# Kernel tuning notes

Hardware: AMD Instinct MI355X
Metric: run time of the kernel (lower is better)

## Reference

```python
import jax, jax.numpy as jnp
import numpy as np

B, S, IN_F, OUT_F, RANK = 4, 4096, 4096, 4096, 64

def soft_threshold24(w):
    # 2:4 soft-threshold pruning: groups of 4 along last dim; keep top-2 |w|,
    # soft-threshold by t = 3rd-largest |w| in each group: sign(w)*relu(|w|-t).
    g = w.reshape(w.shape[0], -1, 4)
    a = jnp.abs(g)
    t = jnp.sort(a, axis=-1)[..., 1:2]  # 3rd largest = 2nd smallest of 4
    s = jnp.sign(g) * jnp.maximum(a - t, 0.0)
    return s.reshape(w.shape)

def fake_fp8_mm(a, b):
    # simulated fp8 GEMM per fake_fp8_mm: fp16 operands, fp32 accumulate/output
    return jnp.matmul(a.astype(jnp.float16), b.astype(jnp.float16),
                      preferred_element_type=jnp.float32)

def setup_inputs():
    key = jax.random.key(0)
    k1, k2, k3 = jax.random.split(key, 3)
    x = jax.random.normal(k1, (B, S, IN_F), jnp.float32)
    std_a = float(np.sqrt(2.0 / (IN_F + RANK)))   # xavier_normal_
    std_b = float(np.sqrt(2.0 / (OUT_F + RANK)))
    weight_A = jax.random.normal(k2, (IN_F, RANK), jnp.float32) * std_a
    weight_B = jax.random.normal(k3, (OUT_F, RANK), jnp.float32) * std_b
    bias = jnp.zeros((OUT_F,), jnp.float32)
    scale_A = jnp.float32(1.0)
    scale_B = jnp.float32(1.0)
    return {"x": x, "weight_A": weight_A, "weight_B": weight_B,
            "bias": bias, "scale_A": scale_A, "scale_B": scale_B}

def reference(x, weight_A, weight_B, bias, scale_A, scale_B):
    wA = soft_threshold24(weight_A) * scale_A      # [IN, R], 2:4 sparse along R
    wB = soft_threshold24(weight_B) * scale_B      # [OUT, R], 2:4 sparse along R
    xf = x.reshape(-1, x.shape[-1])                # [N, IN]
    x_proj = fake_fp8_mm(xf, wA)                   # [N, R]   == FP8SparseOp(x, wA.T, None)
    out = fake_fp8_mm(x_proj, wB.T) + bias         # [N, OUT] == FP8SparseOp(x_proj, wB, bias)
    return out.reshape(*x.shape[:-1], OUT_F)
```

## Files before the change

### kernel.cpp

```cpp
#include <hip/hip_runtime.h>
#include <hip/hip_cooperative_groups.h>

namespace cg = cooperative_groups;

#define IN_FEAT 4096
#define OUT_FEAT 4096
#define RANK 64
#define NROWS 16384
#define TM 32
#define BT 512
#define KC 256
#define WA_STRIDE 264
#define XP_STRIDE 72
#define PART_STRIDE 68

typedef _Float16 half_t;
typedef _Float16 f16x4 __attribute__((ext_vector_type(4)));
typedef _Float16 f16x8 __attribute__((ext_vector_type(8)));
typedef float f32x4 __attribute__((ext_vector_type(4)));

__device__ __forceinline__ f16x4 thr4(float4 v, float s) {
    float a0 = fabsf(v.x), a1 = fabsf(v.y), a2 = fabsf(v.z), a3 = fabsf(v.w);
    float lo1 = fminf(a0, a1), hi1 = fmaxf(a0, a1);
    float lo2 = fminf(a2, a3), hi2 = fmaxf(a2, a3);
    float t = fminf(fmaxf(lo1, lo2), fminf(hi1, hi2));
    f16x4 r;
    r[0] = (half_t)(copysignf(fmaxf(a0 - t, 0.0f), v.x) * s);
    r[1] = (half_t)(copysignf(fmaxf(a1 - t, 0.0f), v.y) * s);
    r[2] = (half_t)(copysignf(fmaxf(a2 - t, 0.0f), v.z) * s);
    r[3] = (half_t)(copysignf(fmaxf(a3 - t, 0.0f), v.w) * s);
    return r;
}

__global__ __launch_bounds__(512) void coop_kernel(
    const float* __restrict__ x, const float* __restrict__ wA,
    const float* __restrict__ wB, const float* __restrict__ bias,
    const float* __restrict__ scaleA, const float* __restrict__ scaleB,
    float* __restrict__ out, half_t* __restrict__ wAT, half_t* __restrict__ wBh)
{
    __shared__ float xp_part[4][TM][PART_STRIDE];
    __shared__ __align__(16) half_t xp[TM][XP_STRIDE];

    int tid = threadIdx.x;
    int bid = blockIdx.x;

    {
        int id = bid * BT + tid;
        if (id < 131072) {
            bool isB = id >= 65536;
            int gid = id & 65535;
            int row = gid >> 4;
            int gq  = gid & 15;
            const float* src = (isB ? wB : wA) + (size_t)row * RANK + gq * 4;
            float s = isB ? scaleB[0] : scaleA[0];
            f16x4 h = thr4(*(const float4*)src, s);
            if (!isB) {
                int c = gq * 4;
                wAT[(size_t)(c + 0) * IN_FEAT + row] = h[0];
                wAT[(size_t)(c + 1) * IN_FEAT + row] = h[1];
                wAT[(size_t)(c + 2) * IN_FEAT + row] = h[2];
                wAT[(size_t)(c + 3) * IN_FEAT + row] = h[3];
            } else {
                *(f16x4*)(wBh + (size_t)row * RANK + gq * 4) = h;
            }
        }
    }
    cg::this_grid().sync();

    int wave = tid >> 6;
    int lane = tid & 63;
    int l16  = lane & 15;
    int g    = lane >> 4;
    int rowbase = bid * TM;
    int stripe  = wave & 1;
    int ks      = wave >> 1;

    {
        const float* xrow = x + (size_t)(rowbase + stripe * 16 + l16) * IN_FEAT;
        int kbeg = ks * (IN_FEAT / 4);
        f32x4 acc[4] = {f32x4{0,0,0,0}, f32x4{0,0,0,0}, f32x4{0,0,0,0}, f32x4{0,0,0,0}};

#pragma unroll 2
        for (int k0 = kbeg; k0 < kbeg + IN_FEAT / 4; k0 += 32) {
            float4 xa = *(const float4*)(xrow + k0 + 8 * g);
            float4 xb = *(const float4*)(xrow + k0 + 8 * g + 4);
            f16x8 a;
            a[0] = (half_t)xa.x; a[1] = (half_t)xa.y; a[2] = (half_t)xa.z; a[3] = (half_t)xa.w;
            a[4] = (half_t)xb.x; a[5] = (half_t)xb.y; a[6] = (half_t)xb.z; a[7] = (half_t)xb.w;
#pragma unroll
            for (int f = 0; f < 4; ++f) {
                f16x8 b = *(const f16x8*)(wAT + (size_t)(16 * f + l16) * IN_FEAT + k0 + 8 * g);
                acc[f] = __builtin_amdgcn_mfma_f32_16x16x32_f16(a, b, acc[f], 0, 0, 0);
            }
        }
#pragma unroll
        for (int f = 0; f < 4; ++f)
#pragma unroll
            for (int r = 0; r < 4; ++r)
                xp_part[ks][stripe * 16 + 4 * g + r][16 * f + l16] = acc[f][r];
    }
    __syncthreads();

#pragma unroll
    for (int i = 0; i < (TM * RANK) / BT; ++i) {
        int e = i * BT + tid;
        int r = e >> 6, c = e & 63;
        xp[r][c] = (half_t)((xp_part[0][r][c] + xp_part[1][r][c]) +
                            (xp_part[2][r][c] + xp_part[3][r][c]));
    }
    __syncthreads();

    {
        const half_t* xprow = &xp[stripe * 16 + l16][0];
        f16x8 a0 = *(const f16x8*)(xprow + 8 * g);
        f16x8 a1 = *(const f16x8*)(xprow + 32 + 8 * g);

        int cb0 = ks * (OUT_FEAT / 4);
        for (int cb = cb0; cb < cb0 + OUT_FEAT / 4; cb += 64) {
#pragma unroll
            for (int f = 0; f < 4; ++f) {
                int col = cb + 16 * f + l16;
                const half_t* wp = wBh + (size_t)col * RANK;
                f16x8 b0 = *(const f16x8*)(wp + 8 * g);
                f16x8 b1 = *(const f16x8*)(wp + 32 + 8 * g);
                f32x4 acc2 = {0, 0, 0, 0};
                acc2 = __builtin_amdgcn_mfma_f32_16x16x32_f16(a0, b0, acc2, 0, 0, 0);
                acc2 = __builtin_amdgcn_mfma_f32_16x16x32_f16(a1, b1, acc2, 0, 0, 0);
                float bv = bias[col];
#pragma unroll
                for (int r = 0; r < 4; ++r)
                    __builtin_nontemporal_store(acc2[r] + bv,
                        &out[(size_t)(rowbase + stripe * 16 + 4 * g + r) * OUT_FEAT + col]);
            }
        }
    }
}

__global__ __launch_bounds__(256) void fused_kernel(
    const float* __restrict__ x, const float* __restrict__ wA,
    const float* __restrict__ wB, const float* __restrict__ bias,
    const float* __restrict__ scaleA, const float* __restrict__ scaleB,
    float* __restrict__ out)
{
    __shared__ __align__(16) half_t wAsT[RANK][WA_STRIDE];
    __shared__ float xp_part[2][TM][XP_STRIDE];
    __shared__ __align__(16) half_t xp[TM][XP_STRIDE];

    int tid  = threadIdx.x;
    int wave = tid >> 6;
    int lane = tid & 63;
    int l16  = lane & 15;
    int g    = lane >> 4;
    int rowbase = blockIdx.x * TM;
    int stripe  = wave & 1;
    int ks      = wave >> 1;

    float sA = scaleA[0];
    float sB = scaleB[0];

    const float* xrow = x + (size_t)(rowbase + stripe * 16 + l16) * IN_FEAT;
    f32x4 acc[4] = {f32x4{0,0,0,0}, f32x4{0,0,0,0}, f32x4{0,0,0,0}, f32x4{0,0,0,0}};

    for (int chunk = 0; chunk < IN_FEAT / KC; ++chunk) {
        int k0 = chunk * KC;
#pragma unroll
        for (int pp = 0; pp < 2; ++pp) {
            int p = tid + pp * 256;
            int q = p & 15;
            int r = p >> 4;
            f16x8 vc0, vc1, vc2, vc3;
#pragma unroll
            for (int i = 0; i < 8; ++i) {
                float4 v = *(const float4*)(wA + (size_t)(k0 + 8 * r + i) * RANK + 4 * q);
                f16x4 h = thr4(v, sA);
                vc0[i] = h[0]; vc1[i] = h[1]; vc2[i] = h[2]; vc3[i] = h[3];
            }
            *(f16x8*)&wAsT[4 * q + 0][8 * r] = vc0;
            *(f16x8*)&wAsT[4 * q + 1][8 * r] = vc1;
            *(f16x8*)&wAsT[4 * q + 2][8 * r] = vc2;
            *(f16x8*)&wAsT[4 * q + 3][8 * r] = vc3;
        }
        __syncthreads();

#pragma unroll
        for (int it = 0; it < 4; ++it) {
            int kloc = ks * 128 + it * 32;
            float4 xa = *(const float4*)(xrow + k0 + kloc + 8 * g);
            float4 xb = *(const float4*)(xrow + k0 + kloc + 8 * g + 4);
            f16x8 a;
            a[0] = (half_t)xa.x; a[1] = (half_t)xa.y; a[2] = (half_t)xa.z; a[3] = (half_t)xa.w;
            a[4] = (half_t)xb.x; a[5] = (half_t)xb.y; a[6] = (half_t)xb.z; a[7] = (half_t)xb.w;
#pragma unroll
            for (int f = 0; f < 4; ++f) {
                f16x8 b = *(const f16x8*)&wAsT[16 * f + l16][kloc + 8 * g];
                acc[f] = __builtin_amdgcn_mfma_f32_16x16x32_f16(a, b, acc[f], 0, 0, 0);
            }
        }
        __syncthreads();
    }

#pragma unroll
    for (int f = 0; f < 4; ++f)
#pragma unroll
        for (int r = 0; r < 4; ++r)
            xp_part[ks][stripe * 16 + 4 * g + r][16 * f + l16] = acc[f][r];
    __syncthreads();

#pragma unroll
    for (int i = 0; i < (TM * RANK) / 256; ++i) {
        int e = i * 256 + tid;
        int r = e >> 6, c = e & 63;
        xp[r][c] = (half_t)(xp_part[0][r][c] + xp_part[1][r][c]);
    }
    __syncthreads();

    {
        const half_t* xprow = &xp[stripe * 16 + l16][0];
        f16x8 a0 = *(const f16x8*)(xprow + 8 * g);
        f16x8 a1 = *(const f16x8*)(xprow + 32 + 8 * g);

        int cb0 = ks * (OUT_FEAT / 2);
        for (int cb = cb0; cb < cb0 + OUT_FEAT / 2; cb += 16) {
            int col = cb + l16;
            const float* wp = wB + (size_t)col * RANK;
            float4 w00 = *(const float4*)(wp + 8 * g);
            float4 w01 = *(const float4*)(wp + 8 * g + 4);
            float4 w10 = *(const float4*)(wp + 32 + 8 * g);
            float4 w11 = *(const float4*)(wp + 32 + 8 * g + 4);
            f16x4 b00 = thr4(w00, sB), b01 = thr4(w01, sB);
            f16x4 b10 = thr4(w10, sB), b11 = thr4(w11, sB);
            f16x8 b0, b1;
            b0[0]=b00[0]; b0[1]=b00[1]; b0[2]=b00[2]; b0[3]=b00[3];
            b0[4]=b01[0]; b0[5]=b01[1]; b0[6]=b01[2]; b0[7]=b01[3];
            b1[0]=b10[0]; b1[1]=b10[1]; b1[2]=b10[2]; b1[3]=b10[3];
            b1[4]=b11[0]; b1[5]=b11[1]; b1[6]=b11[2]; b1[7]=b11[3];

            f32x4 acc2 = {0, 0, 0, 0};
            acc2 = __builtin_amdgcn_mfma_f32_16x16x32_f16(a0, b0, acc2, 0, 0, 0);
            acc2 = __builtin_amdgcn_mfma_f32_16x16x32_f16(a1, b1, acc2, 0, 0, 0);
            float bv = bias[col];
#pragma unroll
            for (int r = 0; r < 4; ++r)
                out[(size_t)(rowbase + stripe * 16 + 4 * g + r) * OUT_FEAT + col] = acc2[r] + bv;
        }
    }
}

extern "C" void kernel_launch(void* const* d_in, const int* in_sizes, int n_in,
                              void* d_out, int out_size, void* d_ws, size_t ws_size,
                              hipStream_t stream) {
    const float* x      = (const float*)d_in[0];
    const float* wA     = (const float*)d_in[1];
    const float* wB     = (const float*)d_in[2];
    const float* bias   = (const float*)d_in[3];
    const float* scaleA = (const float*)d_in[4];
    const float* scaleB = (const float*)d_in[5];
    float* out = (float*)d_out;

    const size_t WS_NEED = (size_t)RANK * IN_FEAT * 2
                         + (size_t)OUT_FEAT * RANK * 2;

    if (ws_size >= WS_NEED && d_ws != nullptr) {
        half_t* wAT = (half_t*)d_ws;
        half_t* wBh = wAT + (size_t)RANK * IN_FEAT;
        void* args[] = {(void*)&x, (void*)&wA, (void*)&wB, (void*)&bias,
                        (void*)&scaleA, (void*)&scaleB, (void*)&out,
                        (void*)&wAT, (void*)&wBh};
        hipLaunchCooperativeKernel((void*)coop_kernel, dim3(NROWS / TM), dim3(BT),
                                   args, 0, stream);
    } else {
        fused_kernel<<<NROWS / TM, 256, 0, stream>>>(x, wA, wB, bias, scaleA, scaleB, out);
    }
}
```

Before: 239.5 us.

## Stage x through double-buffered LDS and split first GEMM by output columns

The first GEMM now loads each x row tile cooperatively into a double-buffered fp16 LDS buffer with register prefetch. Each wave computes one 16-column slice of the rank over the full K range, where before four K-split partials were reduced through LDS. This removes the redundant per-wave global x loads and the fp32 partial reduction. The cost is a block barrier per 256-wide K chunk. The change also swaps nontemporal output stores for plain stores, unrolls the second GEMM loop, and falls back to the non-cooperative kernel if the cooperative launch fails.

```diff
diff --git a/kernel.cpp b/kernel.cpp
--- a/kernel.cpp
+++ b/kernel.cpp
@@ -9,10 +9,11 @@
 #define NROWS 16384
 #define TM 32
 #define BT 512
+#define KC2 256
+#define SXS 264
+#define XP_STRIDE 72
 #define KC 256
 #define WA_STRIDE 264
-#define XP_STRIDE 72
-#define PART_STRIDE 68
 
 typedef _Float16 half_t;
 typedef _Float16 f16x4 __attribute__((ext_vector_type(4)));
@@ -32,13 +33,20 @@
     return r;
 }
 
-__global__ __launch_bounds__(512) void coop_kernel(
+__device__ __forceinline__ f16x4 cvt4(f32x4 v) {
+    f16x4 h;
+    h[0] = (half_t)v[0]; h[1] = (half_t)v[1];
+    h[2] = (half_t)v[2]; h[3] = (half_t)v[3];
+    return h;
+}
+
+__global__ __launch_bounds__(BT) void coop_kernel(
     const float* __restrict__ x, const float* __restrict__ wA,
     const float* __restrict__ wB, const float* __restrict__ bias,
     const float* __restrict__ scaleA, const float* __restrict__ scaleB,
     float* __restrict__ out, half_t* __restrict__ wAT, half_t* __restrict__ wBh)
 {
-    __shared__ float xp_part[4][TM][PART_STRIDE];
+    __shared__ __align__(16) half_t xs[2][TM][SXS];
     __shared__ __align__(16) half_t xp[TM][XP_STRIDE];
 
     int tid = threadIdx.x;
@@ -73,40 +81,57 @@
     int g    = lane >> 4;
     int rowbase = bid * TM;
     int stripe  = wave & 1;
-    int ks      = wave >> 1;
+    int quad    = wave >> 1;
+
+    int srow = tid >> 4;
+    int sseg = tid & 15;
+    const float* srcrow = x + (size_t)(rowbase + srow) * IN_FEAT + sseg * 4;
+
+    f32x4 ld0, ld1, ld2, ld3;
 
     {
-        const float* xrow = x + (size_t)(rowbase + stripe * 16 + l16) * IN_FEAT;
-        int kbeg = ks * (IN_FEAT / 4);
-        f32x4 acc[4] = {f32x4{0,0,0,0}, f32x4{0,0,0,0}, f32x4{0,0,0,0}, f32x4{0,0,0,0}};
-
-#pragma unroll 2
-        for (int k0 = kbeg; k0 < kbeg + IN_FEAT / 4; k0 += 32) {
-            float4 xa = *(const float4*)(xrow + k0 + 8 * g);
-            float4 xb = *(const float4*)(xrow + k0 + 8 * g + 4);
-            f16x8 a;
-            a[0] = (half_t)xa.x; a[1] = (half_t)xa.y; a[2] = (half_t)xa.z; a[3] = (half_t)xa.w;
-            a[4] = (half_t)xb.x; a[5] = (half_t)xb.y; a[6] = (half_t)xb.z; a[7] = (half_t)xb.w;
-#pragma unroll
-            for (int f = 0; f < 4; ++f) {
-                f16x8 b = *(const f16x8*)(wAT + (size_t)(16 * f + l16) * IN_FEAT + k0 + 8 * g);
-                acc[f] = __builtin_amdgcn_mfma_f32_16x16x32_f16(a, b, acc[f], 0, 0, 0);
-            }
-        }
-#pragma unroll
-        for (int f = 0; f < 4; ++f)
-#pragma unroll
-            for (int r = 0; r < 4; ++r)
-                xp_part[ks][stripe * 16 + 4 * g + r][16 * f + l16] = acc[f][r];
-    }
-    __syncthreads();
-
-#pragma unroll
-    for (int i = 0; i < (TM * RANK) / BT; ++i) {
-        int e = i * BT + tid;
-        int r = e >> 6, c = e & 63;
-        xp[r][c] = (half_t)((xp_part[0][r][c] + xp_part[1][r][c]) +
-                            (xp_part[2][r][c] + xp_part[3][r][c]));
+        {
+            const f32x4* p = (const f32x4*)(srcrow);
+            ld0 = p[0]; ld1 = p[16]; ld2 = p[32]; ld3 = p[48];
+            half_t* dst = &xs[0][srow][sseg * 4];
+            *(f16x4*)(dst +   0) = cvt4(ld0);
+            *(f16x4*)(dst +  64) = cvt4(ld1);
+            *(f16x4*)(dst + 128) = cvt4(ld2);
+            *(f16x4*)(dst + 192) = cvt4(ld3);
+        }
+        __syncthreads();
+
+        f32x4 acc = {0, 0, 0, 0};
+        const half_t* wcol = wAT + (size_t)(quad * 16 + l16) * IN_FEAT;
+        const half_t* arow = &xs[0][stripe * 16 + l16][0];
+        const int xsstep = TM * SXS;
+
+        for (int c = 0; c < IN_FEAT / KC2; ++c) {
+            if (c + 1 < IN_FEAT / KC2) {
+                const f32x4* p = (const f32x4*)(srcrow + (c + 1) * KC2);
+                ld0 = p[0]; ld1 = p[16]; ld2 = p[32]; ld3 = p[48];
+            }
+            int kb = c * KC2;
+            const half_t* ar = arow + (c & 1) * xsstep;
+#pragma unroll
+            for (int k8 = 0; k8 < KC2 / 32; ++k8) {
+                f16x8 a = *(const f16x8*)(ar + k8 * 32 + 8 * g);
+                f16x8 b = *(const f16x8*)(wcol + kb + k8 * 32 + 8 * g);
+                acc = __builtin_amdgcn_mfma_f32_16x16x32_f16(a, b, acc, 0, 0, 0);
+            }
+            if (c + 1 < IN_FEAT / KC2) {
+                half_t* dst = &xs[(c + 1) & 1][srow][sseg * 4];
+                *(f16x4*)(dst +   0) = cvt4(ld0);
+                *(f16x4*)(dst +  64) = cvt4(ld1);
+                *(f16x4*)(dst + 128) = cvt4(ld2);
+                *(f16x4*)(dst + 192) = cvt4(ld3);
+            }
+            __syncthreads();
+        }
+
+#pragma unroll
+        for (int r = 0; r < 4; ++r)
+            xp[stripe * 16 + 4 * g + r][quad * 16 + l16] = (half_t)acc[r];
     }
     __syncthreads();
 
@@ -115,7 +140,8 @@
         f16x8 a0 = *(const f16x8*)(xprow + 8 * g);
         f16x8 a1 = *(const f16x8*)(xprow + 32 + 8 * g);
 
-        int cb0 = ks * (OUT_FEAT / 4);
+        int cb0 = quad * (OUT_FEAT / 4);
+#pragma unroll 2
         for (int cb = cb0; cb < cb0 + OUT_FEAT / 4; cb += 64) {
 #pragma unroll
             for (int f = 0; f < 4; ++f) {
@@ -129,8 +155,7 @@
                 float bv = bias[col];
 #pragma unroll
                 for (int r = 0; r < 4; ++r)
-                    __builtin_nontemporal_store(acc2[r] + bv,
-                        &out[(size_t)(rowbase + stripe * 16 + 4 * g + r) * OUT_FEAT + col]);
+                    out[(size_t)(rowbase + stripe * 16 + 4 * g + r) * OUT_FEAT + col] = acc2[r] + bv;
             }
         }
     }
@@ -260,15 +285,19 @@
     const size_t WS_NEED = (size_t)RANK * IN_FEAT * 2
                          + (size_t)OUT_FEAT * RANK * 2;
 
+    bool launched = false;
     if (ws_size >= WS_NEED && d_ws != nullptr) {
         half_t* wAT = (half_t*)d_ws;
         half_t* wBh = wAT + (size_t)RANK * IN_FEAT;
         void* args[] = {(void*)&x, (void*)&wA, (void*)&wB, (void*)&bias,
                         (void*)&scaleA, (void*)&scaleB, (void*)&out,
                         (void*)&wAT, (void*)&wBh};
-        hipLaunchCooperativeKernel((void*)coop_kernel, dim3(NROWS / TM), dim3(BT),
-                                   args, 0, stream);
-    } else {
+        hipError_t err = hipLaunchCooperativeKernel((void*)coop_kernel,
+                                                    dim3(NROWS / TM), dim3(BT),
+                                                    args, 0, stream);
+        launched = (err == hipSuccess);
+    }
+    if (!launched) {
         fused_kernel<<<NROWS / TM, 256, 0, stream>>>(x, wA, wB, bias, scaleA, scaleB, out);
     }
 }
```

Measured after the change: 256.9 us. 7.3% more time.
